# Optimization experiments

Measured on AMD Instinct MI355X. Metric: run time of the kernel, lower is better.

The kernel has to match this reference:

```python
import jax, jax.numpy as jnp
from jax import lax
import numpy as np

FSIZE = 5
NUM_FILTERS = 8


def setup_inputs() -> dict:
    key = jax.random.key(0)
    k1, k2, k3 = jax.random.split(key, 3)
    B, H, W = 8, 1024, 1024
    scale = 1.0 / (FSIZE * FSIZE)  # matches .normal_(0, 1/(fsize*fsize))
    return {
        "mosaick": jax.random.uniform(k1, (B, 1, H, W), dtype=jnp.float32),
        "sel_filts": jax.random.normal(k2, (NUM_FILTERS, FSIZE, FSIZE), dtype=jnp.float32) * scale,
        "green_filts": jax.random.normal(k3, (NUM_FILTERS, FSIZE, FSIZE), dtype=jnp.float32) * scale,
    }


def _conv_bank(x_padded, filts):
    # x_padded: [B,1,H+2p,W+2p], filts: [K,f,f] -> [B,K,H,W]
    return lax.conv_general_dilated(
        x_padded, filts[:, None, :, :], (1, 1), "VALID",
        dimension_numbers=("NCHW", "OIHW", "NCHW"))


def reference(mosaick, sel_filts, green_filts):
    # Space-variant learned demosaicking of the green channel:
    # per-pixel softmax over a bank of selection-filter responses picks a
    # convex combination of candidate green interpolations; known green
    # samples (GRBG: x%2 == y%2) are passed through from the mosaick.
    B, _, H, W = mosaick.shape
    p = FSIZE // 2
    padded = jnp.pad(mosaick, ((0, 0), (0, 0), (p, p), (p, p)), mode="edge")
    sel = _conv_bank(padded, sel_filts)        # [B,K,H,W] selection scores
    interp = _conv_bank(padded, green_filts)   # [B,K,H,W] green candidates
    w = jax.nn.softmax(sel, axis=1)            # per-pixel filter weights
    green_hat = jnp.sum(w * interp, axis=1, keepdims=True)  # [B,1,H,W]
    yy = jnp.arange(H)[:, None]
    xx = jnp.arange(W)[None, :]
    gmask = ((xx % 2) == (yy % 2)).astype(mosaick.dtype)  # GRBG green sites
    green = gmask * mosaick + (1.0 - gmask) * green_hat
    return green  # corresponds to output[:, 1:2, ...]
```

## Files before the change

### kernel.cpp

```cpp
#include <hip/hip_runtime.h>

#define HW_ (1024 * 1024)

typedef _Float16 half8 __attribute__((ext_vector_type(8)));
typedef float f32x4 __attribute__((ext_vector_type(4)));

__global__ __launch_bounds__(256, 2)
void demosaick_mfma(const float* __restrict__ mosaick,
                    const float* __restrict__ sel_filts,
                    const float* __restrict__ green_filts,
                    float* __restrict__ out) {
    __shared__ __align__(16) _Float16 smem[2240];

    const int tid = threadIdx.x;
    const int b   = blockIdx.z;
    const int by0 = blockIdx.y * 32, bx0 = blockIdx.x * 32;
    const float* img = mosaick + (size_t)b * HW_;

    for (int idx = tid; idx < 1440; idx += 256) {
        int row = idx / 40, col = idx - row * 40;
        int gy = by0 - 2 + row; gy = gy < 0 ? 0 : (gy > 1023 ? 1023 : gy);
        int gx = bx0 - 2 + col; gx = gx < 0 ? 0 : (gx > 1023 ? 1023 : gx);
        smem[idx] = (_Float16)img[gy * 1024 + gx];
    }
    for (int idx = tid; idx < 512; idx += 256) {
        int ch = idx >> 5, t = idx & 31;
        float v = 0.f;
        if (t < 25) v = (ch < 8) ? sel_filts[ch * 25 + t]
                                 : green_filts[(ch - 8) * 25 + t];
        smem[1440 + idx] = (_Float16)v;
    }
    for (int idx = tid; idx < 288; idx += 256)
        smem[1952 + idx] = (_Float16)0.f;
    __syncthreads();

    const int lane = tid & 63, w = tid >> 6;
    const int c = lane & 15, q = lane >> 4;

    const half8 afrag = *(const half8*)&smem[1440 + c * 32 + q * 8];

    int b_idx[8];
    #pragma unroll
    for (int j = 0; j < 8; ++j) {
        int t = q * 8 + j;
        int dy = t / 5, dx = t - dy * 5;
        b_idx[j] = (t >= 25) ? 1952 : (w * 320 + dy * 40 + 2 * c + dx);
    }

    float* outp = out + (size_t)b * HW_;
    const float L2E = 1.44269504f;

    #pragma unroll
    for (int g = 0; g < 8; ++g) {
        const int imm = g * 40 + ((g & 1) ? 0 : 1);

        half8 b8;
        #pragma unroll
        for (int j = 0; j < 8; ++j) b8[j] = smem[b_idx[j] + imm];

        f32x4 z = {0.f, 0.f, 0.f, 0.f};
        f32x4 acc = __builtin_amdgcn_mfma_f32_16x16x32_f16(afrag, b8, z, 0, 0, 0);

        float eg = 0.f, se = 0.f;
        #pragma unroll
        for (int r = 0; r < 4; ++r) {
            float goth = __shfl_xor(acc[r], 32);
            float e = __builtin_amdgcn_exp2f(acc[r] * L2E);
            eg = fmaf(e, goth, eg);
            se += e;
        }
        eg += __shfl_xor(eg, 16);
        se += __shfl_xor(se, 16);
        float gh = eg * __builtin_amdgcn_rcpf(se);

        if (q == 0) {
            float pass = (float)smem[(w * 8 + g + 2) * 40 + 2 * c + 2 + (g & 1)];
            float2 o;
            if (g & 1) { o.x = gh;   o.y = pass; }
            else       { o.x = pass; o.y = gh;   }
            int y = by0 + w * 8 + g;
            *(float2*)(outp + (size_t)y * 1024 + bx0 + 2 * c) = o;
        }
    }
}

extern "C" void kernel_launch(void* const* d_in, const int* in_sizes, int n_in,
                              void* d_out, int out_size, void* d_ws, size_t ws_size,
                              hipStream_t stream) {
    const float* mosaick     = (const float*)d_in[0];
    const float* sel_filts   = (const float*)d_in[1];
    const float* green_filts = (const float*)d_in[2];
    float* out = (float*)d_out;
    const int B = in_sizes[0] / HW_;
    dim3 grid(1024 / 32, 1024 / 32, B);
    dim3 block(256, 1, 1);
    hipLaunchKernelGGL(demosaick_mfma, grid, block, 0, stream,
                       mosaick, sel_filts, green_filts, out);
}
```

Measured before the change: 111.1 us.

## Switch to 32x32x16 MFMA with parity-specific filter layout and word-wide B loads

Replaces the 16x16x32 MFMA per row with two 32x32x16 MFMAs per row, using a 16x64 tile. The filter A-matrix is reordered per pixel parity so that the B operand can be assembled from 32-bit LDS word loads instead of eight scalar half loads. Selection and green channels are interleaved so the softmax-weighted sum needs no cross-lane shuffle for pairing, only one xor-32 reduction. The pass-through value is taken from the already-loaded fragment. The tap remapping is intricate, so any mismatch in it would break correctness.

```diff
diff --git a/kernel.cpp b/kernel.cpp
--- a/kernel.cpp
+++ b/kernel.cpp
@@ -3,83 +3,105 @@
 #define HW_ (1024 * 1024)
 
 typedef _Float16 half8 __attribute__((ext_vector_type(8)));
-typedef float f32x4 __attribute__((ext_vector_type(4)));
+typedef float f32x16 __attribute__((ext_vector_type(16)));
+typedef unsigned int uint;
 
 __global__ __launch_bounds__(256, 2)
-void demosaick_mfma(const float* __restrict__ mosaick,
-                    const float* __restrict__ sel_filts,
-                    const float* __restrict__ green_filts,
-                    float* __restrict__ out) {
-    __shared__ __align__(16) _Float16 smem[2240];
+void demosaick_mfma2(const float* __restrict__ mosaick,
+                     const float* __restrict__ sel_filts,
+                     const float* __restrict__ green_filts,
+                     float* __restrict__ out) {
+    __shared__ __align__(16) _Float16 smem[3456];
 
     const int tid = threadIdx.x;
     const int b   = blockIdx.z;
-    const int by0 = blockIdx.y * 32, bx0 = blockIdx.x * 32;
+    const int by0 = blockIdx.y * 16, bx0 = blockIdx.x * 64;
     const float* img = mosaick + (size_t)b * HW_;
 
-    for (int idx = tid; idx < 1440; idx += 256) {
-        int row = idx / 40, col = idx - row * 40;
+    for (int idx = tid; idx < 1360; idx += 256) {
+        int row = idx / 68, col = idx - row * 68;
         int gy = by0 - 2 + row; gy = gy < 0 ? 0 : (gy > 1023 ? 1023 : gy);
         int gx = bx0 - 2 + col; gx = gx < 0 ? 0 : (gx > 1023 ? 1023 : gx);
         smem[idx] = (_Float16)img[gy * 1024 + gx];
     }
-    for (int idx = tid; idx < 512; idx += 256) {
-        int ch = idx >> 5, t = idx & 31;
+    for (int idx = tid; idx < 2048; idx += 256) {
+        int po = idx >> 10, m = (idx >> 5) & 31, kk = idx & 31;
+        int pb = po, sdx = po ? 0 : 4;
+        int dy = -1, dx = 0;
+        if (kk < 16)           { int h = kk >> 3, j = kk & 7;
+                                 dy = 2 * h + (j >> 2); dx = pb + (j & 3); }
+        else if (kk < 18)      { dy = 4; dx = pb + (kk - 16); }
+        else if (kk == 18)     { dy = 0; dx = sdx; }
+        else if (kk == 19)     { dy = 1; dx = sdx; }
+        else if (kk == 20)     { dy = 2; dx = sdx; }
+        else if (kk >= 24 && kk < 26) { dy = 4; dx = pb + 2 + (kk - 24); }
+        else if (kk == 26)     { dy = 3; dx = sdx; }
+        else if (kk == 27)     { dy = 4; dx = sdx; }
         float v = 0.f;
-        if (t < 25) v = (ch < 8) ? sel_filts[ch * 25 + t]
-                                 : green_filts[(ch - 8) * 25 + t];
-        smem[1440 + idx] = (_Float16)v;
+        if (m < 16 && dy >= 0)
+            v = ((m & 1) ? green_filts : sel_filts)[(m >> 1) * 25 + dy * 5 + dx];
+        smem[1360 + idx] = (_Float16)v;
     }
-    for (int idx = tid; idx < 288; idx += 256)
-        smem[1952 + idx] = (_Float16)0.f;
+    for (int idx = tid; idx < 32; idx += 256) smem[3408 + idx] = (_Float16)0.f;
     __syncthreads();
 
     const int lane = tid & 63, w = tid >> 6;
-    const int c = lane & 15, q = lane >> 4;
+    const int n = lane & 31, h = lane >> 5;
 
-    const half8 afrag = *(const half8*)&smem[1440 + c * 32 + q * 8];
+    const half8 a0p0 = *(const half8*)&smem[1360 +        n * 32 + h * 8];
+    const half8 a1p0 = *(const half8*)&smem[1360 +        n * 32 + 16 + h * 8];
+    const half8 a0p1 = *(const half8*)&smem[1360 + 1024 + n * 32 + h * 8];
+    const half8 a1p1 = *(const half8*)&smem[1360 + 1024 + n * 32 + 16 + h * 8];
 
-    int b_idx[8];
-    #pragma unroll
-    for (int j = 0; j < 8; ++j) {
-        int t = q * 8 + j;
-        int dy = t / 5, dx = t - dy * 5;
-        b_idx[j] = (t >= 25) ? 1952 : (w * 320 + dy * 40 + 2 * c + dx);
-    }
-
+    const uint* smw = (const uint*)smem;
+    const unsigned short* sms = (const unsigned short*)smem;
     float* outp = out + (size_t)b * HW_;
     const float L2E = 1.44269504f;
 
     #pragma unroll
-    for (int g = 0; g < 8; ++g) {
-        const int imm = g * 40 + ((g & 1) ? 0 : 1);
+    for (int u = 0; u < 4; ++u) {
+        const int r  = 4 * w + u;
+        const int po = (u & 1) ^ 1;
+        const int pb = po, sdx = po ? 0 : 4;
+        const int e0 = (r + 2 * h) * 68 + 2 * n + po;
+        const int e4 = (r + 4) * 68 + 2 * n + po;
+        const int rs0 = h ? 3 : 0, rs1 = h ? 4 : 1;
 
-        half8 b8;
+        uint B0x = smw[(e0 + pb) >> 1];
+        uint B0y = smw[(e0 + pb + 2) >> 1];
+        uint B0z = smw[(e0 + 68 + pb) >> 1];
+        uint B0w = smw[(e0 + 68 + pb + 2) >> 1];
+        uint B1x = smw[(e4 + pb + 2 * h) >> 1];
+        uint us0 = sms[(r + rs0) * 68 + 2 * n + po + sdx];
+        uint us1 = sms[(r + rs1) * 68 + 2 * n + po + sdx];
+        uint B1y = us0 | (us1 << 16);
+        uint B1z = sms[h ? 3408 : ((r + 2) * 68 + 2 * n + po + sdx)];
+        uint B1w = 0;
+
+        union { uint u4[4]; half8 v; } b0c = {{B0x, B0y, B0z, B0w}};
+        union { uint u4[4]; half8 v; } b1c = {{B1x, B1y, B1z, B1w}};
+
+        f32x16 acc = {};
+        acc = __builtin_amdgcn_mfma_f32_32x32x16_f16(po ? a0p1 : a0p0, b0c.v, acc, 0, 0, 0);
+        acc = __builtin_amdgcn_mfma_f32_32x32x16_f16(po ? a1p1 : a1p0, b1c.v, acc, 0, 0, 0);
+
+        float se = 0.f, eg = 0.f;
         #pragma unroll
-        for (int j = 0; j < 8; ++j) b8[j] = smem[b_idx[j] + imm];
-
-        f32x4 z = {0.f, 0.f, 0.f, 0.f};
-        f32x4 acc = __builtin_amdgcn_mfma_f32_16x16x32_f16(afrag, b8, z, 0, 0, 0);
-
-        float eg = 0.f, se = 0.f;
-        #pragma unroll
-        for (int r = 0; r < 4; ++r) {
-            float goth = __shfl_xor(acc[r], 32);
-            float e = __builtin_amdgcn_exp2f(acc[r] * L2E);
-            eg = fmaf(e, goth, eg);
+        for (int rr = 0; rr < 8; rr += 2) {
+            float e = __builtin_amdgcn_exp2f(acc[rr] * L2E);
             se += e;
+            eg = fmaf(e, acc[rr + 1], eg);
         }
-        eg += __shfl_xor(eg, 16);
-        se += __shfl_xor(se, 16);
+        eg += __shfl_xor(eg, 32);
+        se += __shfl_xor(se, 32);
         float gh = eg * __builtin_amdgcn_rcpf(se);
 
-        if (q == 0) {
-            float pass = (float)smem[(w * 8 + g + 2) * 40 + 2 * c + 2 + (g & 1)];
+        if (h == 1) {
+            float pass = (float)(po ? b0c.v[0] : b0c.v[3]);
             float2 o;
-            if (g & 1) { o.x = gh;   o.y = pass; }
-            else       { o.x = pass; o.y = gh;   }
-            int y = by0 + w * 8 + g;
-            *(float2*)(outp + (size_t)y * 1024 + bx0 + 2 * c) = o;
+            if (po) { o.x = pass; o.y = gh; }
+            else    { o.x = gh;   o.y = pass; }
+            *(float2*)(outp + (size_t)(by0 + r) * 1024 + bx0 + 2 * n) = o;
         }
     }
 }
@@ -92,8 +114,8 @@
     const float* green_filts = (const float*)d_in[2];
     float* out = (float*)d_out;
     const int B = in_sizes[0] / HW_;
-    dim3 grid(1024 / 32, 1024 / 32, B);
+    dim3 grid(1024 / 64, 1024 / 16, B);
     dim3 block(256, 1, 1);
-    hipLaunchKernelGGL(demosaick_mfma, grid, block, 0, stream,
+    hipLaunchKernelGGL(demosaick_mfma2, grid, block, 0, stream,
                        mosaick, sel_filts, green_filts, out);
 }
```

After: 111.9 us. No clear change (+0.6%).
